# Kernel tuning notes

Hardware: AMD Instinct MI355X
Metric: run time of the kernel (lower is better)

The kernel has to match this reference:

```python
import jax, jax.numpy as jnp
import numpy as np

TOP_K = 2


def setup_inputs() -> dict:
    key = jax.random.key(0)
    k1, k2 = jax.random.split(key)
    T, D, E = 16384, 2048, 64
    x = jax.random.normal(k1, (T, D), dtype=jnp.float32)
    W = jax.random.normal(k2, (E, D), dtype=jnp.float32) * 0.02  # gate weight [num_experts, embed_dim]
    return {"x": x, "W": W}


def reference(x, W):
    # gate: logits[t,e] = x[t,:] @ W[e,:]
    logits = jnp.einsum('td,ed->te', x, W)
    probs = jax.nn.softmax(logits, axis=-1)
    # top-k over experts (descending, matches torch.topk)
    top_k_weights, top_k_indices = jax.lax.top_k(probs, TOP_K)
    top_k_weights = top_k_weights / (jnp.sum(top_k_weights, axis=-1, keepdims=True) + 1e-9)
    return (top_k_weights, top_k_indices)
```

## Files before the change

kernel.cpp:

```cpp
#include <hip/hip_runtime.h>
#include <hip/hip_bf16.h>
#include <hip/hip_fp16.h>
#include <math.h>

#define T_TOKENS 16384
#define DDIM 2048
#define NEXP 64
#define REFINE_TAU 4e-3f
#define KSPLIT 8
#define KPW (DDIM / KSPLIT)
#define NCHW (KPW / 32)
#define BLK_TOK 16
#define NBLK (T_TOKENS / BLK_TOK)

typedef _Float16 f16x8 __attribute__((ext_vector_type(8)));
typedef float f32x4 __attribute__((ext_vector_type(4)));

__global__ __launch_bounds__(256)
void prep_w(const float* __restrict__ W, _Float16* __restrict__ pw) {
    const int t  = blockIdx.x * 256 + threadIdx.x;
    const int r  = t >> 8;
    const int kc = (t & 255) * 8;
    const float* wp = &W[(size_t)r * DDIM + kc];
    const float4 a = *(const float4*)wp;
    const float4 b = *(const float4*)(wp + 4);
    const float f[8] = { a.x, a.y, a.z, a.w, b.x, b.y, b.z, b.w };
    f16x8 h;
#pragma unroll
    for (int j = 0; j < 8; ++j) h[j] = (_Float16)f[j];
    const int g = r >> 4, ks = kc >> 5;
    const int lane = (((kc >> 3) & 3) << 4) + (r & 15);
    *(f16x8*)&pw[(((size_t)g * 64 + ks) * 64 + lane) * 8] = h;
}

__device__ __forceinline__ bool better(double va, int ia, double vb, int ib) {
    return (va > vb) || (va == vb && ia < ib);
}

__device__ __forceinline__ double dot_f64_fast(const float* __restrict__ xrow,
                                               const float* __restrict__ wr, int lane) {
    float4 xa[8], wa[8];
#pragma unroll
    for (int q = 0; q < 8; ++q) {
        xa[q] = *(const float4*)&xrow[q * 256 + lane * 4];
        wa[q] = *(const float4*)&wr[q * 256 + lane * 4];
    }
    double s0 = 0.0, s1 = 0.0, s2 = 0.0, s3 = 0.0;
#pragma unroll
    for (int q = 0; q < 8; ++q) {
        s0 = fma((double)xa[q].x, (double)wa[q].x, s0);
        s1 = fma((double)xa[q].y, (double)wa[q].y, s1);
        s2 = fma((double)xa[q].z, (double)wa[q].z, s2);
        s3 = fma((double)xa[q].w, (double)wa[q].w, s3);
    }
    double sd = (s0 + s1) + (s2 + s3);
#pragma unroll
    for (int off = 32; off >= 1; off >>= 1) sd += __shfl_xor(sd, off);
    return sd;
}

#define LOADX(slot, c) do { \
    const float* p_ = xsrc + (size_t)(c) * 32; \
    xr[slot][0] = *(const float4*)p_; \
    xr[slot][1] = *(const float4*)(p_ + 4); \
} while (0)

#define LOADP(buf, c) do { \
    _Pragma("unroll") \
    for (int mt_ = 0; mt_ < 4; ++mt_) \
        pa[buf][mt_] = *(const f16x8*)&pw[pbase + (size_t)(c) * 512 + (size_t)mt_ * 32768]; \
} while (0)

#define CHUNK(slot, buf) do { \
    f16x8 af_; \
    af_[0] = (_Float16)xr[slot][0].x; af_[1] = (_Float16)xr[slot][0].y; \
    af_[2] = (_Float16)xr[slot][0].z; af_[3] = (_Float16)xr[slot][0].w; \
    af_[4] = (_Float16)xr[slot][1].x; af_[5] = (_Float16)xr[slot][1].y; \
    af_[6] = (_Float16)xr[slot][1].z; af_[7] = (_Float16)xr[slot][1].w; \
    _Pragma("unroll") \
    for (int mt_ = 0; mt_ < 4; ++mt_) \
        acc[mt_] = __builtin_amdgcn_mfma_f32_16x16x32_f16(pa[buf][mt_], af_, acc[mt_], 0, 0, 0); \
} while (0)

__global__ __launch_bounds__(512, 4)
void gate_fused(const float* __restrict__ x,
                const _Float16* __restrict__ pw,
                const float* __restrict__ W,
                float* __restrict__ out) {
    __shared__ float part[KSPLIT][NEXP][17];

    const int tid  = threadIdx.x;
    const int lane = tid & 63;
    const int w    = tid >> 6;
    const int tokb = blockIdx.x * BLK_TOK;

    const float* xsrc = x + (size_t)(tokb + (lane & 15)) * DDIM
                          + (size_t)w * KPW + ((lane >> 4) << 3);
    const size_t pbase = (size_t)w * 4096 + (size_t)lane * 8;

    f32x4 acc[4] = { {0,0,0,0}, {0,0,0,0}, {0,0,0,0}, {0,0,0,0} };
    float4 xr[3][2];
    f16x8 pa[2][4];

    LOADX(0, 0); LOADX(1, 1); LOADX(2, 2);
    LOADP(0, 0);

#pragma unroll
    for (int c = 0; c < NCHW; ++c) {
        if (c + 1 < NCHW) LOADP((c + 1) & 1, c + 1);
        CHUNK(c % 3, c & 1);
        if (c + 3 < NCHW) LOADX((c + 3) % 3, c + 3);
    }

#pragma unroll
    for (int mt = 0; mt < 4; ++mt)
#pragma unroll
        for (int j = 0; j < 4; ++j) {
            const int e = mt * 16 + ((lane >> 4) << 2) + j;
            part[w][e][lane & 15] = acc[mt][j];
        }
    __syncthreads();

    float* __restrict__ outw = out;
    float* __restrict__ outi = out + (size_t)T_TOKENS * 2;

#pragma unroll 1
    for (int t = 0; t < 2; ++t) {
        const int lt  = w * 2 + t;
        const int tok = tokb + lt;
        const float l = (((part[0][lane][lt] + part[1][lane][lt])
                        + (part[2][lane][lt] + part[3][lane][lt]))
                       + ((part[4][lane][lt] + part[5][lane][lt])
                        + (part[6][lane][lt] + part[7][lane][lt])));

        float v1 = l; int i1 = lane;
#pragma unroll
        for (int off = 32; off >= 1; off >>= 1) {
            const float ov = __shfl_xor(v1, off);
            const int   oi = __shfl_xor(i1, off);
            if (ov > v1 || (ov == v1 && oi < i1)) { v1 = ov; i1 = oi; }
        }
        float v2 = (lane == i1) ? -INFINITY : l; int i2 = lane;
#pragma unroll
        for (int off = 32; off >= 1; off >>= 1) {
            const float ov = __shfl_xor(v2, off);
            const int   oi = __shfl_xor(i2, off);
            if (ov > v2 || (ov == v2 && oi < i2)) { v2 = ov; i2 = oi; }
        }
        float v3 = (lane == i1 || lane == i2) ? -INFINITY : l; int i3 = lane;
#pragma unroll
        for (int off = 32; off >= 1; off >>= 1) {
            const float ov = __shfl_xor(v3, off);
            const int   oi = __shfl_xor(i3, off);
            if (ov > v3 || (ov == v3 && oi < i3)) { v3 = ov; i3 = oi; }
        }

        const float p = expf(l - v1);
        float s = p;
#pragma unroll
        for (int off = 32; off >= 1; off >>= 1) s += __shfl_xor(s, off);

        int iA = i1, iB = i2;
        if ((v1 - v2) < REFINE_TAU || (v2 - v3) < REFINE_TAU) {
            const float* __restrict__ xrow = x + (size_t)tok * DDIM;
            double La = dot_f64_fast(xrow, W + (size_t)i1 * DDIM, lane);
            double Lb = dot_f64_fast(xrow, W + (size_t)i2 * DDIM, lane);
            double Lc = dot_f64_fast(xrow, W + (size_t)i3 * DDIM, lane);
            int ia = i1, ib = i2, ic = i3;
            if (!better(La, ia, Lb, ib)) { double tv = La; La = Lb; Lb = tv; int ti = ia; ia = ib; ib = ti; }
            if (!better(Lb, ib, Lc, ic)) { double tv = Lb; Lb = Lc; Lc = tv; int ti = ib; ib = ic; ic = ti; }
            if (!better(La, ia, Lb, ib)) { double tv = La; La = Lb; Lb = tv; int ti = ia; ia = ib; ib = ti; }
            iA = ia; iB = ib;
        }

        const float pA = __shfl(p, iA);
        const float pB = __shfl(p, iB);
        const float pa_ = pA / s;
        const float pb_ = pB / s;
        const float inv = 1.0f / (pa_ + pb_ + 1e-9f);

        if (lane == 0) {
            const size_t tg2 = (size_t)tok;
            outw[tg2 * 2]     = pa_ * inv;
            outw[tg2 * 2 + 1] = pb_ * inv;
            outi[tg2 * 2]     = (float)iA;
            outi[tg2 * 2 + 1] = (float)iB;
        }
    }
}

extern "C" void kernel_launch(void* const* d_in, const int* in_sizes, int n_in,
                              void* d_out, int out_size, void* d_ws, size_t ws_size,
                              hipStream_t stream) {
    const float* x = (const float*)d_in[0];
    const float* W = (const float*)d_in[1];
    float* out = (float*)d_out;
    _Float16* pw = (_Float16*)d_ws;

    prep_w<<<NEXP * DDIM / 8 / 256, 256, 0, stream>>>(W, pw);
    gate_fused<<<NBLK, 512, 0, stream>>>(x, pw, W, out);
}
```

Measured before the change: 53.25 us.

## Stage x tiles via global_load_lds and split experts across waves instead of K

Restructures the gate GEMM so each of 4 waves owns 16 experts over the full K dimension, instead of 8 waves each covering a K slice of all experts. x tiles are loaded asynchronously into double-buffered, XOR-swizzled LDS with global_load_lds, which removes the cross-wave partial-sum reduction. Blocks shrink to 256 threads, and each wave handles 4 tokens in the top-k epilogue. The trade-off is a __syncthreads per K chunk and LDS-read conversion overhead, plus fewer waves per block to hide latency.

```diff
diff --git a/kernel.cpp b/kernel.cpp
--- a/kernel.cpp
+++ b/kernel.cpp
@@ -7,14 +7,17 @@
 #define DDIM 2048
 #define NEXP 64
 #define REFINE_TAU 4e-3f
-#define KSPLIT 8
-#define KPW (DDIM / KSPLIT)
-#define NCHW (KPW / 32)
-#define BLK_TOK 16
-#define NBLK (T_TOKENS / BLK_TOK)
+#define NCHK 16
+#define NBLK (T_TOKENS / 16)
 
 typedef _Float16 f16x8 __attribute__((ext_vector_type(8)));
 typedef float f32x4 __attribute__((ext_vector_type(4)));
+
+__device__ __forceinline__ void gload_lds16(const void* g, void* l) {
+    __builtin_amdgcn_global_load_lds(
+        (const __attribute__((address_space(1))) void*)g,
+        (__attribute__((address_space(3))) void*)l, 16, 0, 0);
+}
 
 __global__ __launch_bounds__(256)
 void prep_w(const float* __restrict__ W, _Float16* __restrict__ pw) {
@@ -59,109 +62,113 @@
     return sd;
 }
 
-#define LOADX(slot, c) do { \
-    const float* p_ = xsrc + (size_t)(c) * 32; \
-    xr[slot][0] = *(const float4*)p_; \
-    xr[slot][1] = *(const float4*)(p_ + 4); \
+#define STAGE(buf, c) do { \
+    gload_lds16(xs0 + (size_t)(c) * 512, (char*)&xa[buf][0] + (4 * w)     * 512); \
+    gload_lds16(xs1 + (size_t)(c) * 512, (char*)&xa[buf][0] + (4 * w + 2) * 512); \
 } while (0)
 
 #define LOADP(buf, c) do { \
     _Pragma("unroll") \
-    for (int mt_ = 0; mt_ < 4; ++mt_) \
-        pa[buf][mt_] = *(const f16x8*)&pw[pbase + (size_t)(c) * 512 + (size_t)mt_ * 32768]; \
+    for (int ks_ = 0; ks_ < 4; ++ks_) \
+        pan[buf][ks_] = *(const f16x8*)&pw[(((size_t)w * 64 + (c) * 4 + ks_) * 64 + lane) * 8]; \
 } while (0)
 
-#define CHUNK(slot, buf) do { \
-    f16x8 af_; \
-    af_[0] = (_Float16)xr[slot][0].x; af_[1] = (_Float16)xr[slot][0].y; \
-    af_[2] = (_Float16)xr[slot][0].z; af_[3] = (_Float16)xr[slot][0].w; \
-    af_[4] = (_Float16)xr[slot][1].x; af_[5] = (_Float16)xr[slot][1].y; \
-    af_[6] = (_Float16)xr[slot][1].z; af_[7] = (_Float16)xr[slot][1].w; \
+#define COMPUTE(buf) do { \
     _Pragma("unroll") \
-    for (int mt_ = 0; mt_ < 4; ++mt_) \
-        acc[mt_] = __builtin_amdgcn_mfma_f32_16x16x32_f16(pa[buf][mt_], af_, acc[mt_], 0, 0, 0); \
+    for (int ks_ = 0; ks_ < 4; ++ks_) { \
+        const int col_ = ks_ * 128 + ((lane >> 4) << 5); \
+        const f32x4 v0_ = *(const f32x4*)((const char*)&xa[buf][0] + rbase + ((col_)      ^ rswz)); \
+        const f32x4 v1_ = *(const f32x4*)((const char*)&xa[buf][0] + rbase + ((col_ + 16) ^ rswz)); \
+        f16x8 af_; \
+        af_[0] = (_Float16)v0_[0]; af_[1] = (_Float16)v0_[1]; \
+        af_[2] = (_Float16)v0_[2]; af_[3] = (_Float16)v0_[3]; \
+        af_[4] = (_Float16)v1_[0]; af_[5] = (_Float16)v1_[1]; \
+        af_[6] = (_Float16)v1_[2]; af_[7] = (_Float16)v1_[3]; \
+        acc = __builtin_amdgcn_mfma_f32_16x16x32_f16(pan[buf][ks_], af_, acc, 0, 0, 0); \
+    } \
 } while (0)
 
-__global__ __launch_bounds__(512, 4)
+__global__ __launch_bounds__(256)
 void gate_fused(const float* __restrict__ x,
                 const _Float16* __restrict__ pw,
                 const float* __restrict__ W,
                 float* __restrict__ out) {
-    __shared__ float part[KSPLIT][NEXP][17];
+    __shared__ float xa[2][2048];
+    __shared__ float lg[16][68];
 
     const int tid  = threadIdx.x;
     const int lane = tid & 63;
     const int w    = tid >> 6;
-    const int tokb = blockIdx.x * BLK_TOK;
-
-    const float* xsrc = x + (size_t)(tokb + (lane & 15)) * DDIM
-                          + (size_t)w * KPW + ((lane >> 4) << 3);
-    const size_t pbase = (size_t)w * 4096 + (size_t)lane * 8;
-
-    f32x4 acc[4] = { {0,0,0,0}, {0,0,0,0}, {0,0,0,0}, {0,0,0,0} };
-    float4 xr[3][2];
-    f16x8 pa[2][4];
-
-    LOADX(0, 0); LOADX(1, 1); LOADX(2, 2);
+    const int tokb = blockIdx.x * 16;
+
+    const int r0 = 4 * w + (lane >> 5);
+    const int r1 = 4 * w + 2 + (lane >> 5);
+    const int v0 = ((lane & 31) * 16) ^ ((r0 & 7) << 4);
+    const int v1 = ((lane & 31) * 16) ^ ((r1 & 7) << 4);
+    const char* xs0 = (const char*)x + (size_t)(tokb + r0) * (DDIM * 4) + v0;
+    const char* xs1 = (const char*)x + (size_t)(tokb + r1) * (DDIM * 4) + v1;
+
+    const int rbase = (lane & 15) * 512;
+    const int rswz  = (lane & 7) << 4;
+
+    f16x8 pan[2][4];
+    f32x4 acc = { 0.f, 0.f, 0.f, 0.f };
+
+    STAGE(0, 0);
     LOADP(0, 0);
-
-#pragma unroll
-    for (int c = 0; c < NCHW; ++c) {
-        if (c + 1 < NCHW) LOADP((c + 1) & 1, c + 1);
-        CHUNK(c % 3, c & 1);
-        if (c + 3 < NCHW) LOADX((c + 3) % 3, c + 3);
-    }
-
-#pragma unroll
-    for (int mt = 0; mt < 4; ++mt)
-#pragma unroll
-        for (int j = 0; j < 4; ++j) {
-            const int e = mt * 16 + ((lane >> 4) << 2) + j;
-            part[w][e][lane & 15] = acc[mt][j];
-        }
+    __syncthreads();
+
+#pragma unroll
+    for (int c = 0; c < NCHK; ++c) {
+        if (c + 1 < NCHK) {
+            STAGE((c + 1) & 1, c + 1);
+            LOADP((c + 1) & 1, c + 1);
+        }
+        COMPUTE(c & 1);
+        __syncthreads();
+    }
+
+    *(f32x4*)&lg[lane & 15][w * 16 + ((lane >> 4) << 2)] = acc;
     __syncthreads();
 
     float* __restrict__ outw = out;
     float* __restrict__ outi = out + (size_t)T_TOKENS * 2;
 
 #pragma unroll 1
-    for (int t = 0; t < 2; ++t) {
-        const int lt  = w * 2 + t;
+    for (int t = 0; t < 4; ++t) {
+        const int lt  = w * 4 + t;
         const int tok = tokb + lt;
-        const float l = (((part[0][lane][lt] + part[1][lane][lt])
-                        + (part[2][lane][lt] + part[3][lane][lt]))
-                       + ((part[4][lane][lt] + part[5][lane][lt])
-                        + (part[6][lane][lt] + part[7][lane][lt])));
-
-        float v1 = l; int i1 = lane;
+        const float l = lg[lt][lane];
+
+        float v1v = l; int i1 = lane;
 #pragma unroll
         for (int off = 32; off >= 1; off >>= 1) {
-            const float ov = __shfl_xor(v1, off);
+            const float ov = __shfl_xor(v1v, off);
             const int   oi = __shfl_xor(i1, off);
-            if (ov > v1 || (ov == v1 && oi < i1)) { v1 = ov; i1 = oi; }
-        }
-        float v2 = (lane == i1) ? -INFINITY : l; int i2 = lane;
+            if (ov > v1v || (ov == v1v && oi < i1)) { v1v = ov; i1 = oi; }
+        }
+        float v2v = (lane == i1) ? -INFINITY : l; int i2 = lane;
 #pragma unroll
         for (int off = 32; off >= 1; off >>= 1) {
-            const float ov = __shfl_xor(v2, off);
+            const float ov = __shfl_xor(v2v, off);
             const int   oi = __shfl_xor(i2, off);
-            if (ov > v2 || (ov == v2 && oi < i2)) { v2 = ov; i2 = oi; }
-        }
-        float v3 = (lane == i1 || lane == i2) ? -INFINITY : l; int i3 = lane;
+            if (ov > v2v || (ov == v2v && oi < i2)) { v2v = ov; i2 = oi; }
+        }
+        float v3v = (lane == i1 || lane == i2) ? -INFINITY : l; int i3 = lane;
 #pragma unroll
         for (int off = 32; off >= 1; off >>= 1) {
-            const float ov = __shfl_xor(v3, off);
+            const float ov = __shfl_xor(v3v, off);
             const int   oi = __shfl_xor(i3, off);
-            if (ov > v3 || (ov == v3 && oi < i3)) { v3 = ov; i3 = oi; }
-        }
-
-        const float p = expf(l - v1);
+            if (ov > v3v || (ov == v3v && oi < i3)) { v3v = ov; i3 = oi; }
+        }
+
+        const float p = expf(l - v1v);
         float s = p;
 #pragma unroll
         for (int off = 32; off >= 1; off >>= 1) s += __shfl_xor(s, off);
 
         int iA = i1, iB = i2;
-        if ((v1 - v2) < REFINE_TAU || (v2 - v3) < REFINE_TAU) {
+        if ((v1v - v2v) < REFINE_TAU || (v2v - v3v) < REFINE_TAU) {
             const float* __restrict__ xrow = x + (size_t)tok * DDIM;
             double La = dot_f64_fast(xrow, W + (size_t)i1 * DDIM, lane);
             double Lb = dot_f64_fast(xrow, W + (size_t)i2 * DDIM, lane);
@@ -198,5 +205,5 @@
     _Float16* pw = (_Float16*)d_ws;
 
     prep_w<<<NEXP * DDIM / 8 / 256, 256, 0, stream>>>(W, pw);
-    gate_fused<<<NBLK, 512, 0, stream>>>(x, pw, W, out);
-}
+    gate_fused<<<NBLK, 256, 0, stream>>>(x, pw, W, out);
+}
```

Result: faster. 45.21 us (median of 2 runs) (-15.1%).
